# Performance work log

Hardware: AMD Instinct MI355X
Metric: run time of the kernel (lower is better)

## Reference

```python
import jax, jax.numpy as jnp
import numpy as np

NEG_SLOPE = 0.2
EPS = 1e-16
N_NODES = 50000
N_EDGES = 800000
D_IN = 128
D_E = 64
HEADS = 4
D_OUT = 32


def setup_inputs() -> dict:
    key = jax.random.key(0)
    k1, k2, k3, k4, k5, k6 = jax.random.split(key, 6)
    H = jax.random.normal(k1, (N_NODES, D_IN), dtype=jnp.float32)
    edge_index = jax.random.randint(k2, (2, N_EDGES), 0, N_NODES, dtype=jnp.int64)
    E = jax.random.normal(k3, (N_EDGES, D_E), dtype=jnp.float32)
    # torch nn.Linear weights: [out_features, in_features]
    W = jax.random.normal(k4, (HEADS * D_OUT, D_IN), dtype=jnp.float32) * (1.0 / np.sqrt(D_IN))
    W_e = jax.random.normal(k5, (HEADS * D_OUT, D_E), dtype=jnp.float32) * (1.0 / np.sqrt(D_E))
    att = jax.random.normal(k6, (1, HEADS, D_OUT), dtype=jnp.float32) * 0.1
    return {"H": H, "edge_index": edge_index, "E": E, "W": W, "W_e": W_e, "att": att}


def reference(H, edge_index, E, W, W_e, att):
    n_nodes = H.shape[0]
    # node transform: [N, heads, d_out]
    HT = (H @ W.T).reshape(n_nodes, HEADS, D_OUT)
    src, dst = edge_index[0], edge_index[1]
    # edge transform: [E, heads, d_out]
    ET = (E @ W_e.T).reshape(-1, HEADS, D_OUT)
    alpha_in = HT[src] + HT[dst] + ET              # [E, heads, d_out]
    alpha_in = jax.nn.leaky_relu(alpha_in, NEG_SLOPE)
    alpha = jnp.sum(alpha_in * att, axis=-1)        # [E, heads]
    # segment softmax over incoming edges of each dst node
    a_max = jax.ops.segment_max(alpha, dst, num_segments=n_nodes)   # [N, heads]
    alpha = jnp.exp(alpha - a_max[dst])
    a_sum = jax.ops.segment_sum(alpha, dst, num_segments=n_nodes)   # [N, heads]
    alpha = alpha / (a_sum[dst] + EPS)
    # weighted aggregation of source features
    messages = HT[src] * alpha[:, :, None]          # [E, heads, d_out]
    H_out = jax.ops.segment_sum(messages, dst, num_segments=n_nodes)  # [N, heads, d_out]
    return H_out.reshape(n_nodes, HEADS * D_OUT)    # concat=True
```

## Files before the change

### kernel.cpp

```cpp
#include <hip/hip_runtime.h>

#define N_NODES 50000
#define N_EDGES 800000
#define D_IN    128
#define D_E     64
#define NH      4
#define F_TOT   128
#define NEG_SLOPE 0.2f

typedef __attribute__((ext_vector_type(8))) short short8;
typedef __attribute__((ext_vector_type(4))) float f32x4;

__device__ __forceinline__ short f2bf(float x) {
    unsigned u = __float_as_uint(x);
    u += 0x7FFFu + ((u >> 16) & 1u);
    return (short)(u >> 16);
}

__device__ __forceinline__ int rfl(int x) {
    return __builtin_amdgcn_readfirstlane(x);
}

__global__ __launch_bounds__(256) void k_pre(
    const float* __restrict__ H, const float* __restrict__ W,
    float* __restrict__ HT, const int* __restrict__ EI,
    int* __restrict__ deg)
{
    const int tid = threadIdx.x;
    for (int e = blockIdx.x * 256 + tid; e < N_EDGES; e += gridDim.x * 256)
        atomicAdd(&deg[EI[N_EDGES + e]], 1);

    __shared__ float wt[D_IN * F_TOT];
    for (int i = tid; i < D_IN * F_TOT; i += 256) {
        const int f = i & 127, k = i >> 7;
        wt[k * F_TOT + f] = W[f * D_IN + k];
    }
    __syncthreads();

    const int l = tid & 63;
    const int w = tid >> 6;
    const int gwave  = blockIdx.x * 4 + w;
    const int nwaves = gridDim.x * 4;
    const int ngroups = N_NODES / 8;

    for (int grp = gwave; grp < ngroups; grp += nwaves) {
        const int g = grp * 8;
        float ax[8], ay[8];
#pragma unroll
        for (int j = 0; j < 8; ++j) { ax[j] = 0.f; ay[j] = 0.f; }

        for (int k4 = 0; k4 < D_IN / 4; ++k4) {
            float hv[8][4];
#pragma unroll
            for (int j = 0; j < 8; ++j)
                *(float4*)hv[j] = *(const float4*)&H[(size_t)(g + j) * D_IN + k4 * 4];
#pragma unroll
            for (int kk = 0; kk < 4; ++kk) {
                const float2 wk = *(const float2*)&wt[(k4 * 4 + kk) * F_TOT + 2 * l];
#pragma unroll
                for (int j = 0; j < 8; ++j) {
                    ax[j] = fmaf(wk.x, hv[j][kk], ax[j]);
                    ay[j] = fmaf(wk.y, hv[j][kk], ay[j]);
                }
            }
        }
#pragma unroll
        for (int j = 0; j < 8; ++j) {
            float2 r; r.x = ax[j]; r.y = ay[j];
            *(float2*)&HT[(size_t)(g + j) * F_TOT + 2 * l] = r;
        }
    }
}

__global__ __launch_bounds__(1024) void k_scan(
    const int* __restrict__ deg, int* __restrict__ row_start,
    int* __restrict__ cursor)
{
    __shared__ int wsum[16];
    __shared__ int carry;
    const int tid = threadIdx.x;
    const int l = tid & 63;
    const int wv = tid >> 6;
    if (tid == 0) carry = 0;

    const int4* deg4 = (const int4*)deg;
    const int N4 = N_NODES / 4;

    for (int base = 0; base < N4; base += 1024) {
        __syncthreads();
        const int cb = carry;
        const int i4 = base + tid;
        int4 d = make_int4(0, 0, 0, 0);
        if (i4 < N4) d = deg4[i4];
        const int t0 = d.x, t1 = t0 + d.y, t2 = t1 + d.z, t3 = t2 + d.w;
        int x = t3;
#pragma unroll
        for (int off = 1; off < 64; off <<= 1) {
            int t = __shfl_up(x, off, 64);
            if (l >= off) x += t;
        }
        if (l == 63) wsum[wv] = x;
        __syncthreads();
        int s = (l < 16) ? wsum[l] : 0;
#pragma unroll
        for (int off = 1; off < 16; off <<= 1) {
            int t = __shfl_up(s, off, 64);
            if (l >= off) s += t;
        }
        const int tot      = __shfl(s, 15, 64);
        const int wave_off = (wv == 0) ? 0 : __shfl(s, wv - 1, 64);
        const int excl     = cb + wave_off + (x - t3);
        if (i4 < N4) {
            int4 rs;
            rs.x = excl; rs.y = excl + t0; rs.z = excl + t1; rs.w = excl + t2;
            ((int4*)row_start)[i4] = rs;
            ((int4*)cursor)[i4]    = rs;
        }
        if (tid == 0) carry = cb + tot;
    }
    __syncthreads();
    if (tid == 0) row_start[N_NODES] = carry;
}

__global__ __launch_bounds__(256) void k_permute(
    const int* __restrict__ EI, int* __restrict__ cursor,
    int2* __restrict__ perm)
{
    const int e = blockIdx.x * 256 + threadIdx.x;
    if (e < N_EDGES) {
        const int src = EI[e];
        const int dst = EI[N_EDGES + e];
        const int pos = atomicAdd(&cursor[dst], 1);
        perm[pos] = make_int2(e, src);
    }
}

__global__ __launch_bounds__(256, 2) void k_fused(
    const float* __restrict__ E, const float* __restrict__ We,
    const float* __restrict__ att, const float* __restrict__ HT,
    const int2* __restrict__ perm, const int* __restrict__ row_start,
    float* __restrict__ out)
{
    __shared__ short8 s_bf[8][2][64];
    __shared__ f32x4  s_att[8][4];
    __shared__ f32x4  s_hd[4][8][4];

    const int tid = threadIdx.x;
    const int l   = tid & 63;
    const int wv  = tid >> 6;
    const int r16 = l & 15;
    const int g4  = l >> 4;

    if (wv == 0) {
#pragma unroll
        for (int ft = 0; ft < 8; ++ft) {
#pragma unroll
            for (int kc = 0; kc < 2; ++kc) {
                const float* wp = &We[(size_t)(ft * 16 + r16) * D_E + kc * 32 + g4 * 8];
                const f32x4 lo = *(const f32x4*)wp;
                const f32x4 hi = *(const f32x4*)(wp + 4);
                short8 b;
                b[0] = f2bf(lo[0]); b[1] = f2bf(lo[1]); b[2] = f2bf(lo[2]); b[3] = f2bf(lo[3]);
                b[4] = f2bf(hi[0]); b[5] = f2bf(hi[1]); b[6] = f2bf(hi[2]); b[7] = f2bf(hi[3]);
                s_bf[ft][kc][l] = b;
            }
        }
        if (l < 32) {
            const int ft = l >> 2, g = l & 3;
            s_att[ft][g] = *(const f32x4*)&att[ft * 16 + g * 4];
        }
    }
    __syncthreads();

    const int gs = rfl(gridDim.x * 4);

    int n0 = rfl(blockIdx.x * 4 + wv);
    int t0 = rfl(row_start[n0]);
    int e0 = rfl(row_start[n0 + 1]);

    int n1 = n0, t1, e1;
    if (t0 + 16 < e0) { t1 = t0 + 16; e1 = e0; }
    else {
        n1 = n0 + gs;
        if (n1 < N_NODES) { t1 = rfl(row_start[n1]); e1 = rfl(row_start[n1 + 1]); }
        else { t1 = 0; e1 = 0; }
    }
    int n2 = n1, t2, e2;
    if (t1 + 16 < e1) { t2 = t1 + 16; e2 = e1; }
    else if (n1 < N_NODES) {
        n2 = n1 + gs;
        if (n2 < N_NODES) { t2 = rfl(row_start[n2]); e2 = rfl(row_start[n2 + 1]); }
        else { t2 = 0; e2 = 0; }
    } else { t2 = 0; e2 = 0; }

    int nN = n2 + gs;
    int bN = 0, eN = 0;
    if (nN < N_NODES) { bN = rfl(row_start[nN]); eN = rfl(row_start[nN + 1]); }

#define PCLAMP(T, EE) (max(min((T) + r16, (EE) - 1), 0))

    int2 pe0v = perm[PCLAMP(t0, e0)];
    int2 pe1v = perm[PCLAMP(t1, e1)];
    int2 pe2v = perm[PCLAMP(t2, e2)];

    f32x4 ev0, ev1, ev2, ev3;
    {
        const float* ep = &E[(size_t)pe0v.x * D_E + g4 * 8];
        ev0 = *(const f32x4*)ep;       ev1 = *(const f32x4*)(ep + 4);
        ev2 = *(const f32x4*)(ep + 32); ev3 = *(const f32x4*)(ep + 36);
    }
    f32x4 hsv[8];
    {
        const float* hp = &HT[(size_t)pe0v.y * F_TOT + g4 * 4];
#pragma unroll
        for (int ft = 0; ft < 8; ++ft) hsv[ft] = *(const f32x4*)(hp + ft * 16);
    }
    if (l < 32 && n0 < N_NODES)
        s_hd[wv][l >> 2][l & 3] = *(const f32x4*)&HT[(size_t)n0 * F_TOT + l * 4];

    f32x4 am[8];
#pragma unroll
    for (int ft = 0; ft < 8; ++ft) am[ft] = (f32x4){0.f, 0.f, 0.f, 0.f};
    float sw[4] = {0.f, 0.f, 0.f, 0.f};
    f32x4 hdld = (f32x4){0.f, 0.f, 0.f, 0.f};

    int safety = 65536;
    while (n0 < N_NODES && safety-- > 0) {
        int n2n = n2, t2n = t2, e2n = e2;
        if (t2 + 16 < e2) { t2n = t2 + 16; }
        else if (n2 < N_NODES) {
            n2n = nN;
            if (nN < N_NODES) { t2n = bN; e2n = eN; } else { t2n = 0; e2n = 0; }
            nN += gs;
            if (nN < N_NODES) { bN = rfl(row_start[nN]); eN = rfl(row_start[nN + 1]); }
        }
        int2 peT = perm[PCLAMP(t2n, e2n)];
        if (l < 32 && n1 < N_NODES)
            hdld = *(const f32x4*)&HT[(size_t)n1 * F_TOT + l * 4];

        short8 af0, af1;
        af0[0]=f2bf(ev0[0]); af0[1]=f2bf(ev0[1]); af0[2]=f2bf(ev0[2]); af0[3]=f2bf(ev0[3]);
        af0[4]=f2bf(ev1[0]); af0[5]=f2bf(ev1[1]); af0[6]=f2bf(ev1[2]); af0[7]=f2bf(ev1[3]);
        af1[0]=f2bf(ev2[0]); af1[1]=f2bf(ev2[1]); af1[2]=f2bf(ev2[2]); af1[3]=f2bf(ev2[3]);
        af1[4]=f2bf(ev3[0]); af1[5]=f2bf(ev3[1]); af1[6]=f2bf(ev3[2]); af1[7]=f2bf(ev3[3]);
        {
            const float* ep = &E[(size_t)pe1v.x * D_E + g4 * 8];
            ev0 = *(const f32x4*)ep;       ev1 = *(const f32x4*)(ep + 4);
            ev2 = *(const f32x4*)(ep + 32); ev3 = *(const f32x4*)(ep + 36);
        }

        float ph[4] = {0.f, 0.f, 0.f, 0.f};
#pragma unroll
        for (int ft = 0; ft < 8; ++ft) {
            f32x4 z = {0.f, 0.f, 0.f, 0.f};
            z = __builtin_amdgcn_mfma_f32_16x16x32_bf16(s_bf[ft][0][l], af0, z, 0, 0, 0);
            const f32x4 acc =
                __builtin_amdgcn_mfma_f32_16x16x32_bf16(s_bf[ft][1][l], af1, z, 0, 0, 0);
            const f32x4 at = s_att[ft][g4];
            const f32x4 hd = s_hd[wv][ft][g4];
#pragma unroll
            for (int r = 0; r < 4; ++r) {
                float v = hsv[ft][r] + hd[r] + acc[r];
                v = v > 0.f ? v : NEG_SLOPE * v;
                ph[ft >> 1] = fmaf(v, at[r], ph[ft >> 1]);
            }
        }
        const bool valid = (t0 + r16) < e0;
#pragma unroll
        for (int h = 0; h < 4; ++h) {
            ph[h] += __shfl_xor(ph[h], 16, 64);
            ph[h] += __shfl_xor(ph[h], 32, 64);
        }
        float w[4];
#pragma unroll
        for (int h = 0; h < 4; ++h) {
            w[h] = valid ? __expf(ph[h]) : 0.f;
            sw[h] += w[h];
        }
#pragma unroll
        for (int ft = 0; ft < 8; ++ft) {
            const float wh = w[ft >> 1];
#pragma unroll
            for (int r = 0; r < 4; ++r)
                am[ft][r] = fmaf(wh, hsv[ft][r], am[ft][r]);
        }
        {
            const float* hp = &HT[(size_t)pe1v.y * F_TOT + g4 * 4];
#pragma unroll
            for (int ft = 0; ft < 8; ++ft) hsv[ft] = *(const f32x4*)(hp + ft * 16);
        }

        if (n1 != n0) {
#pragma unroll
            for (int m = 1; m < 16; m <<= 1) {
#pragma unroll
                for (int h = 0; h < 4; ++h) sw[h] += __shfl_xor(sw[h], m, 64);
#pragma unroll
                for (int ft = 0; ft < 8; ++ft)
#pragma unroll
                    for (int r = 0; r < 4; ++r)
                        am[ft][r] += __shfl_xor(am[ft][r], m, 64);
            }
            float inv[4];
#pragma unroll
            for (int h = 0; h < 4; ++h) inv[h] = 1.f / (sw[h] + 1e-16f);
            if (r16 == 0) {
#pragma unroll
                for (int ft = 0; ft < 8; ++ft) {
                    f32x4 o;
#pragma unroll
                    for (int r = 0; r < 4; ++r) o[r] = am[ft][r] * inv[ft >> 1];
                    *(f32x4*)&out[(size_t)n0 * F_TOT + ft * 16 + g4 * 4] = o;
                }
            }
#pragma unroll
            for (int ft = 0; ft < 8; ++ft) am[ft] = (f32x4){0.f, 0.f, 0.f, 0.f};
            sw[0] = sw[1] = sw[2] = sw[3] = 0.f;
        }
        if (l < 32) s_hd[wv][l >> 2][l & 3] = hdld;

        n0 = n1; t0 = t1; e0 = e1;
        n1 = n2; t1 = t2; e1 = e2;
        n2 = n2n; t2 = t2n; e2 = e2n;
        pe1v = pe2v; pe2v = peT;
    }
#undef PCLAMP
}

extern "C" void kernel_launch(void* const* d_in, const int* in_sizes, int n_in,
                              void* d_out, int out_size, void* d_ws, size_t ws_size,
                              hipStream_t stream)
{
    const float* H   = (const float*)d_in[0];
    const int*   EI  = (const int*)d_in[1];
    const float* E   = (const float*)d_in[2];
    const float* W   = (const float*)d_in[3];
    const float* We  = (const float*)d_in[4];
    const float* att = (const float*)d_in[5];
    float* out = (float*)d_out;

    float* HT        = (float*)d_ws;
    int2*  perm      = (int2*)(HT + (size_t)N_NODES * F_TOT);
    int*   deg       = (int*)(perm + N_EDGES);
    int*   row_start = deg + N_NODES;
    int*   cursor    = row_start + N_NODES + 4;

    hipMemsetAsync(deg, 0, N_NODES * sizeof(int), stream);

    k_pre<<<512, 256, 0, stream>>>(H, W, HT, EI, deg);
    k_scan<<<1, 1024, 0, stream>>>(deg, row_start, cursor);
    k_permute<<<(N_EDGES + 255) / 256, 256, 0, stream>>>(EI, cursor, perm);
    k_fused<<<1024, 256, 0, stream>>>(E, We, att, HT, perm, row_start, out);
}
```

Before: 560.7 us.

## Store node transform in bf16 with permuted layout and deepen edge prefetch

The node feature table HT is now written in bf16 with a permuted column layout, so each lane can fetch its gathered source row with 16-byte loads at half the bytes. The fused kernel deepens the software pipeline by one stage, prefetching edge features two iterations ahead with a double buffer and tracking an extra perm entry. The goal is to cut gather bandwidth and hide the latency of random E row loads. In exchange it adds bf16 rounding error to the messages and aggregated output, and raises register pressure.

New measurement: 568.4 us. No clear change (+1.4%).

```diff
diff --git a/kernel.cpp b/kernel.cpp
--- a/kernel.cpp
+++ b/kernel.cpp
@@ -9,6 +9,7 @@
 #define NEG_SLOPE 0.2f
 
 typedef __attribute__((ext_vector_type(8))) short short8;
+typedef __attribute__((ext_vector_type(8))) unsigned short ushort8;
 typedef __attribute__((ext_vector_type(4))) float f32x4;
 
 __device__ __forceinline__ short f2bf(float x) {
@@ -16,14 +17,17 @@
     u += 0x7FFFu + ((u >> 16) & 1u);
     return (short)(u >> 16);
 }
-
+__device__ __forceinline__ float b2f(unsigned short u) {
+    return __uint_as_float(((unsigned)u) << 16);
+}
 __device__ __forceinline__ int rfl(int x) {
     return __builtin_amdgcn_readfirstlane(x);
 }
 
+
 __global__ __launch_bounds__(256) void k_pre(
     const float* __restrict__ H, const float* __restrict__ W,
-    float* __restrict__ HT, const int* __restrict__ EI,
+    unsigned short* __restrict__ HT16, const int* __restrict__ EI,
     int* __restrict__ deg)
 {
     const int tid = threadIdx.x;
@@ -43,6 +47,9 @@
     const int nwaves = gridDim.x * 4;
     const int ngroups = N_NODES / 8;
 
+    const int f_ = 2 * l;
+    const int pos = (((f_ >> 2) & 3) * 32) + ((f_ >> 4) * 4) + (f_ & 3);
+
     for (int grp = gwave; grp < ngroups; grp += nwaves) {
         const int g = grp * 8;
         float ax[8], ay[8];
@@ -66,8 +73,9 @@
         }
 #pragma unroll
         for (int j = 0; j < 8; ++j) {
-            float2 r; r.x = ax[j]; r.y = ay[j];
-            *(float2*)&HT[(size_t)(g + j) * F_TOT + 2 * l] = r;
+            const unsigned packed = (unsigned)(unsigned short)f2bf(ax[j])
+                                  | ((unsigned)(unsigned short)f2bf(ay[j]) << 16);
+            *(unsigned*)&HT16[(size_t)(g + j) * F_TOT + pos] = packed;
         }
     }
 }
@@ -137,7 +145,7 @@
 
 __global__ __launch_bounds__(256, 2) void k_fused(
     const float* __restrict__ E, const float* __restrict__ We,
-    const float* __restrict__ att, const float* __restrict__ HT,
+    const float* __restrict__ att, const unsigned short* __restrict__ HT16,
     const int2* __restrict__ perm, const int* __restrict__ row_start,
     float* __restrict__ out)
 {
@@ -174,26 +182,23 @@
 
     const int gs = rfl(gridDim.x * 4);
 
+#define ADVP(NI, TI, EI_, NO, TO, EO)                                         \
+    NO = NI;                                                                  \
+    if ((TI) + 16 < (EI_)) { TO = (TI) + 16; EO = (EI_); }                    \
+    else {                                                                    \
+        NO = (NI) + gs;                                                       \
+        if (NO < N_NODES) { TO = rfl(row_start[NO]); EO = rfl(row_start[NO + 1]); } \
+        else { TO = 0; EO = 0; }                                              \
+    }
+
     int n0 = rfl(blockIdx.x * 4 + wv);
     int t0 = rfl(row_start[n0]);
     int e0 = rfl(row_start[n0 + 1]);
-
-    int n1 = n0, t1, e1;
-    if (t0 + 16 < e0) { t1 = t0 + 16; e1 = e0; }
-    else {
-        n1 = n0 + gs;
-        if (n1 < N_NODES) { t1 = rfl(row_start[n1]); e1 = rfl(row_start[n1 + 1]); }
-        else { t1 = 0; e1 = 0; }
-    }
-    int n2 = n1, t2, e2;
-    if (t1 + 16 < e1) { t2 = t1 + 16; e2 = e1; }
-    else if (n1 < N_NODES) {
-        n2 = n1 + gs;
-        if (n2 < N_NODES) { t2 = rfl(row_start[n2]); e2 = rfl(row_start[n2 + 1]); }
-        else { t2 = 0; e2 = 0; }
-    } else { t2 = 0; e2 = 0; }
-
-    int nN = n2 + gs;
+    int n1, t1, e1; ADVP(n0, t0, e0, n1, t1, e1);
+    int n2, t2, e2; ADVP(n1, t1, e1, n2, t2, e2);
+    int n3, t3, e3; ADVP(n2, t2, e2, n3, t3, e3);
+
+    int nN = n3 + gs;
     int bN = 0, eN = 0;
     if (nN < N_NODES) { bN = rfl(row_start[nN]); eN = rfl(row_start[nN + 1]); }
 
@@ -202,51 +207,64 @@
     int2 pe0v = perm[PCLAMP(t0, e0)];
     int2 pe1v = perm[PCLAMP(t1, e1)];
     int2 pe2v = perm[PCLAMP(t2, e2)];
-
-    f32x4 ev0, ev1, ev2, ev3;
+    int2 pe3v = perm[PCLAMP(t3, e3)];
+
+    f32x4 evA0, evA1, evA2, evA3;
+    f32x4 evB0, evB1, evB2, evB3;
     {
         const float* ep = &E[(size_t)pe0v.x * D_E + g4 * 8];
-        ev0 = *(const f32x4*)ep;       ev1 = *(const f32x4*)(ep + 4);
-        ev2 = *(const f32x4*)(ep + 32); ev3 = *(const f32x4*)(ep + 36);
-    }
-    f32x4 hsv[8];
+        evA0 = *(const f32x4*)ep;        evA1 = *(const f32x4*)(ep + 4);
+        evA2 = *(const f32x4*)(ep + 32); evA3 = *(const f32x4*)(ep + 36);
+    }
     {
-        const float* hp = &HT[(size_t)pe0v.y * F_TOT + g4 * 4];
-#pragma unroll
-        for (int ft = 0; ft < 8; ++ft) hsv[ft] = *(const f32x4*)(hp + ft * 16);
-    }
-    if (l < 32 && n0 < N_NODES)
-        s_hd[wv][l >> 2][l & 3] = *(const f32x4*)&HT[(size_t)n0 * F_TOT + l * 4];
+        const float* ep = &E[(size_t)pe1v.x * D_E + g4 * 8];
+        evB0 = *(const f32x4*)ep;        evB1 = *(const f32x4*)(ep + 4);
+        evB2 = *(const f32x4*)(ep + 32); evB3 = *(const f32x4*)(ep + 36);
+    }
+    ushort8 hsv[4];
+    {
+        const unsigned short* hp = &HT16[(size_t)pe0v.y * F_TOT + g4 * 32];
+        hsv[0] = *(const ushort8*)hp;        hsv[1] = *(const ushort8*)(hp + 8);
+        hsv[2] = *(const ushort8*)(hp + 16); hsv[3] = *(const ushort8*)(hp + 24);
+    }
+    if (l < 16 && n0 < N_NODES) {
+        const ushort8 h8 = *(const ushort8*)&HT16[(size_t)n0 * F_TOT + l * 8];
+        f32x4 lo, hi;
+#pragma unroll
+        for (int r = 0; r < 4; ++r) { lo[r] = b2f(h8[r]); hi[r] = b2f(h8[4 + r]); }
+        s_hd[wv][2 * (l & 3)][l >> 2]     = lo;
+        s_hd[wv][2 * (l & 3) + 1][l >> 2] = hi;
+    }
 
     f32x4 am[8];
 #pragma unroll
     for (int ft = 0; ft < 8; ++ft) am[ft] = (f32x4){0.f, 0.f, 0.f, 0.f};
     float sw[4] = {0.f, 0.f, 0.f, 0.f};
-    f32x4 hdld = (f32x4){0.f, 0.f, 0.f, 0.f};
+    ushort8 hdld = (ushort8){0, 0, 0, 0, 0, 0, 0, 0};
 
     int safety = 65536;
     while (n0 < N_NODES && safety-- > 0) {
-        int n2n = n2, t2n = t2, e2n = e2;
-        if (t2 + 16 < e2) { t2n = t2 + 16; }
-        else if (n2 < N_NODES) {
-            n2n = nN;
-            if (nN < N_NODES) { t2n = bN; e2n = eN; } else { t2n = 0; e2n = 0; }
+        int n3n = n3, t3n = t3, e3n = e3;
+        if (t3 + 16 < e3) { t3n = t3 + 16; }
+        else if (n3 < N_NODES) {
+            n3n = nN;
+            if (nN < N_NODES) { t3n = bN; e3n = eN; } else { t3n = 0; e3n = 0; }
             nN += gs;
             if (nN < N_NODES) { bN = rfl(row_start[nN]); eN = rfl(row_start[nN + 1]); }
         }
-        int2 peT = perm[PCLAMP(t2n, e2n)];
-        if (l < 32 && n1 < N_NODES)
-            hdld = *(const f32x4*)&HT[(size_t)n1 * F_TOT + l * 4];
+        int2 peT = perm[PCLAMP(t3n, e3n)];
+        if (l < 16 && n1 < N_NODES)
+            hdld = *(const ushort8*)&HT16[(size_t)n1 * F_TOT + l * 8];
 
         short8 af0, af1;
-        af0[0]=f2bf(ev0[0]); af0[1]=f2bf(ev0[1]); af0[2]=f2bf(ev0[2]); af0[3]=f2bf(ev0[3]);
-        af0[4]=f2bf(ev1[0]); af0[5]=f2bf(ev1[1]); af0[6]=f2bf(ev1[2]); af0[7]=f2bf(ev1[3]);
-        af1[0]=f2bf(ev2[0]); af1[1]=f2bf(ev2[1]); af1[2]=f2bf(ev2[2]); af1[3]=f2bf(ev2[3]);
-        af1[4]=f2bf(ev3[0]); af1[5]=f2bf(ev3[1]); af1[6]=f2bf(ev3[2]); af1[7]=f2bf(ev3[3]);
+        af0[0]=f2bf(evA0[0]); af0[1]=f2bf(evA0[1]); af0[2]=f2bf(evA0[2]); af0[3]=f2bf(evA0[3]);
+        af0[4]=f2bf(evA1[0]); af0[5]=f2bf(evA1[1]); af0[6]=f2bf(evA1[2]); af0[7]=f2bf(evA1[3]);
+        af1[0]=f2bf(evA2[0]); af1[1]=f2bf(evA2[1]); af1[2]=f2bf(evA2[2]); af1[3]=f2bf(evA2[3]);
+        af1[4]=f2bf(evA3[0]); af1[5]=f2bf(evA3[1]); af1[6]=f2bf(evA3[2]); af1[7]=f2bf(evA3[3]);
         {
-            const float* ep = &E[(size_t)pe1v.x * D_E + g4 * 8];
-            ev0 = *(const f32x4*)ep;       ev1 = *(const f32x4*)(ep + 4);
-            ev2 = *(const f32x4*)(ep + 32); ev3 = *(const f32x4*)(ep + 36);
+            const float* ep = &E[(size_t)pe2v.x * D_E + g4 * 8];
+            evA0 = *(const f32x4*)ep;        evA1 = *(const f32x4*)(ep + 4);
+            evA2 = *(const f32x4*)(ep + 32); evA3 = *(const f32x4*)(ep + 36);
         }
 
         float ph[4] = {0.f, 0.f, 0.f, 0.f};
@@ -258,9 +276,11 @@
                 __builtin_amdgcn_mfma_f32_16x16x32_bf16(s_bf[ft][1][l], af1, z, 0, 0, 0);
             const f32x4 at = s_att[ft][g4];
             const f32x4 hd = s_hd[wv][ft][g4];
+            const ushort8 hc = hsv[ft >> 1];
+            const int b = (ft & 1) * 4;
 #pragma unroll
             for (int r = 0; r < 4; ++r) {
-                float v = hsv[ft][r] + hd[r] + acc[r];
+                float v = b2f(hc[b + r]) + hd[r] + acc[r];
                 v = v > 0.f ? v : NEG_SLOPE * v;
                 ph[ft >> 1] = fmaf(v, at[r], ph[ft >> 1]);
             }
@@ -279,15 +299,17 @@
         }
 #pragma unroll
         for (int ft = 0; ft < 8; ++ft) {
+            const ushort8 hc = hsv[ft >> 1];
+            const int b = (ft & 1) * 4;
             const float wh = w[ft >> 1];
 #pragma unroll
             for (int r = 0; r < 4; ++r)
-                am[ft][r] = fmaf(wh, hsv[ft][r], am[ft][r]);
+                am[ft][r] = fmaf(wh, b2f(hc[b + r]), am[ft][r]);
         }
         {
-            const float* hp = &HT[(size_t)pe1v.y * F_TOT + g4 * 4];
-#pragma unroll
-            for (int ft = 0; ft < 8; ++ft) hsv[ft] = *(const f32x4*)(hp + ft * 16);
+            const unsigned short* hp = &HT16[(size_t)pe1v.y * F_TOT + g4 * 32];
+            hsv[0] = *(const ushort8*)hp;        hsv[1] = *(const ushort8*)(hp + 8);
+            hsv[2] = *(const ushort8*)(hp + 16); hsv[3] = *(const ushort8*)(hp + 24);
         }
 
         if (n1 != n0) {
@@ -317,14 +339,27 @@
             for (int ft = 0; ft < 8; ++ft) am[ft] = (f32x4){0.f, 0.f, 0.f, 0.f};
             sw[0] = sw[1] = sw[2] = sw[3] = 0.f;
         }
-        if (l < 32) s_hd[wv][l >> 2][l & 3] = hdld;
+        if (l < 16) {
+            f32x4 lo, hi;
+#pragma unroll
+            for (int r = 0; r < 4; ++r) { lo[r] = b2f(hdld[r]); hi[r] = b2f(hdld[4 + r]); }
+            s_hd[wv][2 * (l & 3)][l >> 2]     = lo;
+            s_hd[wv][2 * (l & 3) + 1][l >> 2] = hi;
+        }
 
         n0 = n1; t0 = t1; e0 = e1;
         n1 = n2; t1 = t2; e1 = e2;
-        n2 = n2n; t2 = t2n; e2 = e2n;
-        pe1v = pe2v; pe2v = peT;
+        n2 = n3; t2 = t3; e2 = e3;
+        n3 = n3n; t3 = t3n; e3 = e3n;
+        pe1v = pe2v; pe2v = pe3v; pe3v = peT;
+        f32x4 tv;
+        tv = evA0; evA0 = evB0; evB0 = tv;
+        tv = evA1; evA1 = evB1; evB1 = tv;
+        tv = evA2; evA2 = evB2; evB2 = tv;
+        tv = evA3; evA3 = evB3; evB3 = tv;
     }
 #undef PCLAMP
+#undef ADVP
 }
 
 extern "C" void kernel_launch(void* const* d_in, const int* in_sizes, int n_in,
@@ -339,16 +374,16 @@
     const float* att = (const float*)d_in[5];
     float* out = (float*)d_out;
 
-    float* HT        = (float*)d_ws;
-    int2*  perm      = (int2*)(HT + (size_t)N_NODES * F_TOT);
-    int*   deg       = (int*)(perm + N_EDGES);
-    int*   row_start = deg + N_NODES;
-    int*   cursor    = row_start + N_NODES + 4;
+    unsigned short* HT16 = (unsigned short*)d_ws;
+    int2* perm      = (int2*)(HT16 + (size_t)N_NODES * F_TOT);
+    int*  deg       = (int*)(perm + N_EDGES);
+    int*  row_start = deg + N_NODES;
+    int*  cursor    = row_start + N_NODES + 4;
 
     hipMemsetAsync(deg, 0, N_NODES * sizeof(int), stream);
 
-    k_pre<<<512, 256, 0, stream>>>(H, W, HT, EI, deg);
+    k_pre<<<512, 256, 0, stream>>>(H, W, HT16, EI, deg);
     k_scan<<<1, 1024, 0, stream>>>(deg, row_start, cursor);
     k_permute<<<(N_EDGES + 255) / 256, 256, 0, stream>>>(EI, cursor, perm);
-    k_fused<<<1024, 256, 0, stream>>>(E, We, att, HT, perm, row_start, out);
-}
+    k_fused<<<1024, 256, 0, stream>>>(E, We, att, HT16, perm, row_start, out);
+}
```
